# Kernel tuning notes

Measured on AMD Instinct MI355X. Metric: run time of the kernel, lower is better.

The kernel has to match this reference:

```python
import jax, jax.numpy as jnp
import numpy as np

B = 65536  # batch size

def setup_inputs() -> dict:
    key = jax.random.key(0)
    ks = jax.random.split(key, 6)
    x = jax.random.normal(ks[0], (B, 784), dtype=jnp.float32)
    conv_w = jax.random.normal(ks[1], (3, 3), dtype=jnp.float32) * 0.1
    in_size = (28 - 3 + 1) * (28 - 3 + 1)  # 676
    w1 = jax.random.normal(ks[2], (in_size, 300), dtype=jnp.float32) * 0.05
    b1 = jax.random.normal(ks[3], (300,), dtype=jnp.float32) * 0.05
    w2 = jax.random.normal(ks[4], (300, 10), dtype=jnp.float32) * 0.05
    b2 = jax.random.normal(ks[5], (10,), dtype=jnp.float32) * 0.05
    return {"x": x, "conv_w": conv_w, "w1": w1, "b1": b1, "w2": w2, "b2": b2}

def _convolve(img, conv_w):
    # img: [B,28,28]; conv_w: [kh,kw]. Valid cross-correlation (tensordot of each
    # window with the un-flipped kernel), matching the original Convolve().
    out = jax.lax.conv_general_dilated(
        img[:, None, :, :],            # [B,1,28,28]  NCHW
        conv_w[None, None, :, :],      # [1,1,3,3]    OIHW (no flip -> cross-correlation)
        window_strides=(1, 1),
        padding="VALID",
        dimension_numbers=("NCHW", "OIHW", "NCHW"),
    )
    return out[:, 0]  # [B,26,26]

def reference(x, conv_w, w1, b1, w2, b2):
    b = x.shape[0]
    img = x.reshape(b, 28, 28)
    feat = _convolve(img, conv_w).reshape(b, -1)      # [B,676]
    h1 = jax.nn.relu(feat @ w1 + b1)                  # [B,300]
    return h1 @ w2 + b2                               # [B,10]
```

## Files before the change

kernel.cpp:

```cpp
#include <hip/hip_runtime.h>
#include <hip/hip_bf16.h>

typedef __attribute__((ext_vector_type(8))) short bf16x8;
typedef __attribute__((ext_vector_type(4))) float f32x4;
typedef __attribute__((ext_vector_type(4))) unsigned int u32x4;
typedef unsigned short u16;
typedef unsigned int u32;

static constexpr int KDIM  = 784;
static constexpr int KP    = 800;
static constexpr int NDIM  = 300;
static constexpr int NP    = 320;
static constexpr int DDIM  = 10;
static constexpr int BM    = 256;
static constexpr int BK    = 32;
static constexpr int NSTEP = 25;
static constexpr int H1STR = 328;
static constexpr int NROW  = 65536;
static constexpr int NTHR  = 512;
static constexpr int ABYTES = 32768;
static constexpr int BBYTES = 20480;
static constexpr int BBASE  = 98304;

__device__ __forceinline__ u16 f2bf(float f) {
  unsigned u = __builtin_bit_cast(unsigned, f);
  u += 0x7fffu + ((u >> 16) & 1u);
  return (u16)(u >> 16);
}
__device__ __forceinline__ u32 pk2(float a, float b) {
  u32 r;
  asm("v_cvt_pk_bf16_f32 %0, %1, %2" : "=v"(r) : "v"(a), "v"(b));
  return r;
}
__device__ __forceinline__ void gll16(const void* g, void* l) {
  __builtin_amdgcn_global_load_lds(
      (const __attribute__((address_space(1))) void*)g,
      (__attribute__((address_space(3))) void*)l, 16, 0, 0);
}

__global__ void build_weff(const float* __restrict__ cw,
                           const float* __restrict__ w1,
                           u16* __restrict__ weff) {
  int idx = blockIdx.x * 256 + threadIdx.x;
  if (idx >= NP * KP) return;
  int n = idx / KP;
  int k = idx - n * KP;
  float acc = 0.f;
  if (n < NDIM && k < KDIM) {
    int r = k / 28, c = k - (k / 28) * 28;
    #pragma unroll
    for (int dr = 0; dr < 3; ++dr) {
      int orr = r - dr;
      if ((unsigned)orr < 26u) {
        #pragma unroll
        for (int dc = 0; dc < 3; ++dc) {
          int oc = c - dc;
          if ((unsigned)oc < 26u)
            acc += cw[dr * 3 + dc] * w1[(orr * 26 + oc) * NDIM + n];
        }
      }
    }
  }
  weff[n * KP + k] = f2bf(acc);
}

__global__ void __launch_bounds__(NTHR, 2)
fused_mlp(const float* __restrict__ x, const float* __restrict__ b1,
          const float* __restrict__ w2, const float* __restrict__ b2,
          const u16* __restrict__ weff, float* __restrict__ out) {
  __shared__ __align__(16) u16 lds[69632];

  const int tid  = threadIdx.x;
  const int wv   = tid >> 6;
  const int lane = tid & 63;
  const int l16  = lane & 15;
  const int lhi  = lane >> 4;
  const int wm   = wv >> 2;
  const int wn   = wv & 3;
  const int bm   = blockIdx.x * BM;
  const int wvn  = wn * 80;

  int aRow[4], aQg[4];
  #pragma unroll
  for (int it = 0; it < 4; ++it) {
    int s = tid + it * NTHR;
    aRow[it] = s >> 3;
    aQg[it]  = (s & 7) ^ (aRow[it] & 7);
  }
  int bRow[3], bQg[3];
  #pragma unroll
  for (int i = 0; i < 3; ++i) {
    int s = (i < 2) ? (tid + i * NTHR) : (1024 + (tid & 255));
    bRow[i] = s >> 2;
    bQg[i]  = (s & 3) ^ (bRow[i] & 3);
  }

  auto stageA = [&](int bufi, int t) {
    char* base = (char*)lds + bufi * ABYTES;
    int k0 = (t < NSTEP) ? t * BK : 0;
    #pragma unroll
    for (int it = 0; it < 4; ++it) {
      int kof = k0 + aQg[it] * 4;
      if (kof >= KDIM) kof = aQg[it] * 4;
      gll16(x + (size_t)(bm + aRow[it]) * KDIM + kof,
            base + (tid + it * NTHR) * 16);
    }
  };
  auto stageB = [&](int bufi, int t) {
    char* base = (char*)lds + BBASE + bufi * BBYTES;
    int k0 = (t < NSTEP) ? t * BK : 0;
    #pragma unroll
    for (int i = 0; i < 3; ++i) {
      int s = (i < 2) ? (tid + i * NTHR) : (1024 + (tid & 255));
      gll16(weff + (size_t)bRow[i] * KP + k0 + bQg[i] * 8, base + s * 16);
    }
  };

  f32x4 acc[8][5];
  #pragma unroll
  for (int mi = 0; mi < 8; ++mi)
    #pragma unroll
    for (int ni = 0; ni < 5; ++ni)
      acc[mi][ni] = (f32x4){0.f, 0.f, 0.f, 0.f};

  auto compute = [&](int abufi, int bbufi) {
    const f32x4* Af = (const f32x4*)((char*)lds + abufi * ABYTES);
    const u16*   Bb = (const u16*)((char*)lds + BBASE + bbufi * BBYTES);
    bf16x8 bfr[5];
    #pragma unroll
    for (int ni = 0; ni < 5; ++ni) {
      int n = wvn + ni * 16 + l16;
      int slot = n * 4 + (lhi ^ (n & 3));
      bfr[ni] = *reinterpret_cast<const bf16x8*>(Bb + slot * 8);
    }
    #pragma unroll
    for (int mi = 0; mi < 8; ++mi) {
      int R = wm * 128 + mi * 16 + l16;
      f32x4 a0 = Af[R * 8 + ((2 * lhi)     ^ (R & 7))];
      f32x4 a1 = Af[R * 8 + ((2 * lhi + 1) ^ (R & 7))];
      u32x4 amu = { pk2(a0[0], a0[1]), pk2(a0[2], a0[3]),
                    pk2(a1[0], a1[1]), pk2(a1[2], a1[3]) };
      bf16x8 am = __builtin_bit_cast(bf16x8, amu);
      #pragma unroll
      for (int ni = 0; ni < 5; ++ni)
        acc[mi][ni] = __builtin_amdgcn_mfma_f32_16x16x32_bf16(am, bfr[ni], acc[mi][ni], 0, 0, 0);
    }
  };

  stageA(0, 0);
  stageB(0, 0);
  stageA(1, 1);
  asm volatile("s_waitcnt vmcnt(4)" ::: "memory");
  __builtin_amdgcn_s_barrier();
  __builtin_amdgcn_sched_barrier(0);

  for (int t = 0; t < NSTEP; ++t) {
    stageB((t + 1) & 1, t + 1);
    stageA((t + 2) % 3, t + 2);
    __builtin_amdgcn_sched_barrier(0);
    compute(t % 3, t & 1);
    __builtin_amdgcn_sched_barrier(0);
    asm volatile("s_waitcnt vmcnt(4)" ::: "memory");
    __builtin_amdgcn_s_barrier();
    __builtin_amdgcn_sched_barrier(0);
  }
  __syncthreads();

  u16* H1  = lds;
  u16* W2T = lds + 20992;

  for (int i = tid; i < 16 * NP; i += NTHR) {
    int d = i / NP, n = i - (i / NP) * NP;
    float v = (d < DDIM && n < NDIM) ? w2[n * DDIM + d] : 0.f;
    W2T[d * H1STR + n] = f2bf(v);
  }
  float biasv[5];
  #pragma unroll
  for (int ni = 0; ni < 5; ++ni) {
    int col = wvn + ni * 16 + l16;
    biasv[ni] = (col < NDIM) ? b1[col] : 0.f;
  }

  #pragma unroll
  for (int p = 0; p < 4; ++p) {
    if (wm == (p >> 1)) {
      #pragma unroll
      for (int mj = 0; mj < 4; ++mj) {
        int mi = (p & 1) * 4 + mj;
        #pragma unroll
        for (int ni = 0; ni < 5; ++ni) {
          int col = wvn + ni * 16 + l16;
          int rb  = mj * 16 + lhi * 4;
          #pragma unroll
          for (int r = 0; r < 4; ++r) {
            float h = acc[mi][ni][r] + biasv[ni];
            H1[(rb + r) * H1STR + col] = f2bf(fmaxf(h, 0.f));
          }
        }
      }
    }
    __syncthreads();
    if (wv < 4) {
      f32x4 a2c = (f32x4){0.f, 0.f, 0.f, 0.f};
      #pragma unroll
      for (int ks = 0; ks < NP / 32; ++ks) {
        bf16x8 a2 = *reinterpret_cast<const bf16x8*>(
            H1 + (wv * 16 + l16) * H1STR + ks * 32 + lhi * 8);
        bf16x8 bw = *reinterpret_cast<const bf16x8*>(
            W2T + l16 * H1STR + ks * 32 + lhi * 8);
        a2c = __builtin_amdgcn_mfma_f32_16x16x32_bf16(a2, bw, a2c, 0, 0, 0);
      }
      if (l16 < DDIM) {
        float bb = b2[l16];
        #pragma unroll
        for (int r = 0; r < 4; ++r) {
          int row = bm + p * 64 + wv * 16 + lhi * 4 + r;
          out[(size_t)row * DDIM + l16] = a2c[r] + bb;
        }
      }
    }
    __syncthreads();
  }
}

extern "C" void kernel_launch(void* const* d_in, const int* in_sizes, int n_in,
                              void* d_out, int out_size, void* d_ws, size_t ws_size,
                              hipStream_t stream) {
  const float* x  = (const float*)d_in[0];
  const float* cw = (const float*)d_in[1];
  const float* w1 = (const float*)d_in[2];
  const float* b1 = (const float*)d_in[3];
  const float* w2 = (const float*)d_in[4];
  const float* b2 = (const float*)d_in[5];
  float* out = (float*)d_out;
  u16* weff = (u16*)d_ws;

  hipLaunchKernelGGL(build_weff, dim3((NP * KP + 255) / 256), dim3(256), 0, stream,
                     cw, w1, weff);
  hipLaunchKernelGGL(fused_mlp, dim3(NROW / BM), dim3(NTHR), 0, stream,
                     x, b1, w2, b2, weff, out);
}
```

Measured before the change: 61.70 us.

## Split K-step compute into four phases with barrier-synced ping-pong and setprio

```diff
diff --git a/kernel.cpp b/kernel.cpp
--- a/kernel.cpp
+++ b/kernel.cpp
@@ -123,30 +123,6 @@
     for (int ni = 0; ni < 5; ++ni)
       acc[mi][ni] = (f32x4){0.f, 0.f, 0.f, 0.f};
 
-  auto compute = [&](int abufi, int bbufi) {
-    const f32x4* Af = (const f32x4*)((char*)lds + abufi * ABYTES);
-    const u16*   Bb = (const u16*)((char*)lds + BBASE + bbufi * BBYTES);
-    bf16x8 bfr[5];
-    #pragma unroll
-    for (int ni = 0; ni < 5; ++ni) {
-      int n = wvn + ni * 16 + l16;
-      int slot = n * 4 + (lhi ^ (n & 3));
-      bfr[ni] = *reinterpret_cast<const bf16x8*>(Bb + slot * 8);
-    }
-    #pragma unroll
-    for (int mi = 0; mi < 8; ++mi) {
-      int R = wm * 128 + mi * 16 + l16;
-      f32x4 a0 = Af[R * 8 + ((2 * lhi)     ^ (R & 7))];
-      f32x4 a1 = Af[R * 8 + ((2 * lhi + 1) ^ (R & 7))];
-      u32x4 amu = { pk2(a0[0], a0[1]), pk2(a0[2], a0[3]),
-                    pk2(a1[0], a1[1]), pk2(a1[2], a1[3]) };
-      bf16x8 am = __builtin_bit_cast(bf16x8, amu);
-      #pragma unroll
-      for (int ni = 0; ni < 5; ++ni)
-        acc[mi][ni] = __builtin_amdgcn_mfma_f32_16x16x32_bf16(am, bfr[ni], acc[mi][ni], 0, 0, 0);
-    }
-  };
-
   stageA(0, 0);
   stageB(0, 0);
   stageA(1, 1);
@@ -155,14 +131,51 @@
   __builtin_amdgcn_sched_barrier(0);
 
   for (int t = 0; t < NSTEP; ++t) {
-    stageB((t + 1) & 1, t + 1);
-    stageA((t + 2) % 3, t + 2);
-    __builtin_amdgcn_sched_barrier(0);
-    compute(t % 3, t & 1);
-    __builtin_amdgcn_sched_barrier(0);
-    asm volatile("s_waitcnt vmcnt(4)" ::: "memory");
-    __builtin_amdgcn_s_barrier();
-    __builtin_amdgcn_sched_barrier(0);
+    const f32x4* Af = (const f32x4*)((char*)lds + (t % 3) * ABYTES);
+    const u16*   Bb = (const u16*)((char*)lds + BBASE + (t & 1) * BBYTES);
+    bf16x8 bfr[5];
+
+    #pragma unroll
+    for (int p = 0; p < 4; ++p) {
+      f32x4 ra0[2], ra1[2];
+      #pragma unroll
+      for (int j = 0; j < 2; ++j) {
+        int R = wm * 128 + (2 * p + j) * 16 + l16;
+        ra0[j] = Af[R * 8 + ((2 * lhi)     ^ (R & 7))];
+        ra1[j] = Af[R * 8 + ((2 * lhi + 1) ^ (R & 7))];
+      }
+      if (p == 0) {
+        #pragma unroll
+        for (int ni = 0; ni < 5; ++ni) {
+          int n = wvn + ni * 16 + l16;
+          bfr[ni] = *reinterpret_cast<const bf16x8*>(Bb + (n * 4 + (lhi ^ (n & 3))) * 8);
+        }
+        stageB((t + 1) & 1, t + 1);
+      }
+      if (p == 1)
+        stageA((t + 2) % 3, t + 2);
+      __builtin_amdgcn_sched_barrier(0);
+      __builtin_amdgcn_s_barrier();
+      asm volatile("s_waitcnt lgkmcnt(0)" ::: "memory");
+      __builtin_amdgcn_sched_barrier(0);
+      __builtin_amdgcn_s_setprio(1);
+      #pragma unroll
+      for (int j = 0; j < 2; ++j) {
+        u32x4 amu = { pk2(ra0[j][0], ra0[j][1]), pk2(ra0[j][2], ra0[j][3]),
+                      pk2(ra1[j][0], ra1[j][1]), pk2(ra1[j][2], ra1[j][3]) };
+        bf16x8 am = __builtin_bit_cast(bf16x8, amu);
+        #pragma unroll
+        for (int ni = 0; ni < 5; ++ni)
+          acc[2 * p + j][ni] =
+              __builtin_amdgcn_mfma_f32_16x16x32_bf16(am, bfr[ni], acc[2 * p + j][ni], 0, 0, 0);
+      }
+      __builtin_amdgcn_s_setprio(0);
+      __builtin_amdgcn_sched_barrier(0);
+      if (p == 3)
+        asm volatile("s_waitcnt vmcnt(4)" ::: "memory");
+      __builtin_amdgcn_s_barrier();
+      __builtin_amdgcn_sched_barrier(0);
+    }
   }
   __syncthreads();
 
```

New measurement: 70.90 us. 14.9% more time.
